# Kernel optimization log

Hardware: AMD Instinct MI355X
Metric: run time of the kernel (lower is better)

The kernel has to match this reference:

```python
import jax, jax.numpy as jnp
import numpy as np

DEPTH = 2
EPS = 1e-12

def _l2norm(x, axis=-1):
    n = jnp.sqrt(jnp.sum(x * x, axis=axis, keepdims=True))
    return x / jnp.maximum(n, EPS)

def setup_inputs() -> dict:
    key = jax.random.key(0)
    k1, k2, k3, k4, k5 = jax.random.split(key, 5)
    N, D, R, E = 50000, 100, 1000, 800000
    features = jax.random.normal(k1, (N, D), dtype=jnp.float32)
    rel_emb = jax.random.normal(k2, (R, D), dtype=jnp.float32)
    none_relation = jax.random.normal(k3, (D,), dtype=jnp.float32)
    # edge list sorted by destination row (matches coalesced sparse layout
    # assumed by the original: softmax values align with edge order)
    rows = jnp.sort(jax.random.randint(k4, (E,), 0, N))
    cols = jax.random.randint(k5, (E,), 0, N)
    adj_index = jnp.stack([rows, cols], axis=1).astype(jnp.int64)
    return {"features": features, "rel_emb": rel_emb,
            "adj_index": adj_index, "none_relation": none_relation}

def reference(features, rel_emb, adj_index, none_relation):
    N = features.shape[0]
    rows = adj_index[:, 0]  # destination (softmax segment, scatter target)
    cols = adj_index[:, 1]  # neighbor (gather source)
    feats = jnp.tanh(features)
    outputs = [feats]
    nr = _l2norm(none_relation, axis=0)  # [D]
    for _ in range(DEPTH):
        neighs = feats[cols]                      # [E, D] gather
        score = -jnp.einsum('ed,d->e', _l2norm(neighs), nr)  # [E]
        # sparse softmax over each destination row's edges
        m = jax.ops.segment_max(score, rows, num_segments=N)
        e = jnp.exp(score - m[rows])
        denom = jax.ops.segment_sum(e, rows, num_segments=N)
        att = e / denom[rows]                     # [E]
        new_feats = jax.ops.segment_sum(neighs * att[:, None], rows,
                                        num_segments=N)  # [N, D]
        feats = jnp.tanh(new_feats)
        outputs.append(feats)
    return jnp.concatenate(outputs, axis=1)  # [N, D*(DEPTH+1)]
```

## Files before the change

kernel.cpp:

```cpp
#include <hip/hip_runtime.h>
#include <hip/hip_fp16.h>
#include <math.h>

#define D_FEAT 100
#define ROW_STRIDE 300
#define ROWB 128u

__device__ __forceinline__ float fast_tanh(float x) {
    float ax = fabsf(x);
    float e  = __expf(2.f * ax);
    float t  = 1.f - 2.f / (e + 1.f);
    return copysignf(t, x);
}

__device__ __forceinline__ unsigned pb4(float x0, float x1, float x2, float x3) {
    unsigned b0 = (unsigned)(int)rintf(fmaf(x0, 127.f, 128.f));
    unsigned b1 = (unsigned)(int)rintf(fmaf(x1, 127.f, 128.f));
    unsigned b2 = (unsigned)(int)rintf(fmaf(x2, 127.f, 128.f));
    unsigned b3 = (unsigned)(int)rintf(fmaf(x3, 127.f, 128.f));
    return b0 | (b1 << 8) | (b2 << 16) | (b3 << 24);
}

__device__ __forceinline__ float half_reduce(float v) {
    #pragma unroll
    for (int off = 16; off; off >>= 1) v += __shfl_xor(v, off, 64);
    return v;
}

__global__ __launch_bounds__(256) void tanh_score_kernel(
    const float* __restrict__ features,
    float* __restrict__ out,
    unsigned char* __restrict__ tab0,
    float* __restrict__ escore0,
    const float* __restrict__ none_rel,
    const int* __restrict__ adj,
    int* __restrict__ startArr,
    int* __restrict__ cols,
    int E, int N)
{
    int gtid = blockIdx.x * blockDim.x + threadIdx.x;
    if (cols && gtid < (E >> 1)) {
        uint4 v = ((const uint4*)adj)[gtid];
        ((int2*)cols)[gtid] = make_int2((int)v.y, (int)v.w);
    }
    if (gtid <= N) {
        if (gtid == N) startArr[N] = E;
        else {
            int lo = 0, hi = E;
            while (lo < hi) {
                int mid = (lo + hi) >> 1;
                if (adj[2 * mid] < gtid) lo = mid + 1; else hi = mid;
            }
            startArr[gtid] = lo;
        }
    }
    if (tab0 && gtid < 8) {
        uint4 z = make_uint4(0x80808080u, 0x80808080u, 0x80808080u, 0x80808080u);
        if (gtid == 7) z.x = 0u;
        *(uint4*)(tab0 + (((size_t)N) << 7) + ((size_t)gtid << 4)) = z;
    }

    int waveId = gtid >> 6;
    int lane = threadIdx.x & 63;
    int h32  = lane >> 5;
    int l    = lane & 31;
    int n    = waveId * 2 + h32;
    const bool valid_n = (n < N);
    const bool fact = valid_n && (l >= 1) && (l <= 25);

    float x0 = 0.f, x1 = 0.f, x2 = 0.f, x3 = 0.f;
    if (fact) {
        float4 f = ((const float4*)(features + (size_t)n * D_FEAT))[l - 1];
        x0 = fast_tanh(f.x); x1 = fast_tanh(f.y);
        x2 = fast_tanh(f.z); x3 = fast_tanh(f.w);
        ((float4*)(out + (size_t)n * ROW_STRIDE))[l - 1] = make_float4(x0, x1, x2, x3);
    }
    unsigned char* row = tab0 ? (tab0 + ((size_t)n << 7)) : nullptr;
    if (row && valid_n) {
        if (l >= 1 && l <= 25) {
            *(unsigned*)(row + 4 * (l - 1)) = pb4(x0, x1, x2, x3);
        } else if (l >= 26 && l != 29) {
            *(unsigned*)(row + 4 * (l - 1)) = 0x80808080u;
        } else if (l == 0) {
            *(unsigned*)(row + 124) = 0x80808080u;
        }
    }

    float nx = 0.f, ny = 0.f, nz = 0.f, nw = 0.f;
    if (l >= 1 && l <= 25) {
        float4 v = ((const float4*)none_rel)[l - 1];
        nx = v.x; ny = v.y; nz = v.z; nw = v.w;
    }
    float ss = half_reduce(nx * nx + ny * ny + nz * nz + nw * nw);
    float inv_nr = 1.f / fmaxf(sqrtf(ss), 1e-12f);

    float dot = half_reduce(x0 * nx + x1 * ny + x2 * nz + x3 * nw) * inv_nr;
    float sq  = half_reduce(x0 * x0 + x1 * x1 + x2 * x2 + x3 * x3);
    if (l == 0 && valid_n) {
        float es = __expf(-dot / fmaxf(sqrtf(sq), 1e-12f));
        escore0[n] = es;
        if (row) *(float*)(row + 112) = es;
    }
}

template <bool WRITE_TAB>
__global__ __launch_bounds__(256) void attn8_kernel(
    const unsigned char* __restrict__ tab,
    float* __restrict__ outp,
    unsigned char* __restrict__ tab_out,
    const int* __restrict__ cols,
    const int* __restrict__ start,
    const float* __restrict__ none_rel,
    int N)
{
    if constexpr (WRITE_TAB) {
        if (blockIdx.x == 0 && threadIdx.x < 8) {
            uint4 z = make_uint4(0x80808080u, 0x80808080u, 0x80808080u, 0x80808080u);
            if (threadIdx.x == 7) z.x = 0u;
            *(uint4*)(tab_out + (((size_t)N) << 7) + ((size_t)threadIdx.x << 4)) = z;
        }
    }

    const int waveId = (int)((blockIdx.x * blockDim.x + threadIdx.x) >> 6);
    const int lane = threadIdx.x & 63;
    const int h32  = lane >> 5;
    const int hl   = lane & 31;
    const int base = h32 << 5;
    const int n    = waveId * 2 + h32;
    const bool valid_n = (n < N);

    const int grp   = hl >> 3;
    const int chunk = hl & 7;
    const unsigned suboff = (unsigned)(chunk << 4);
    const int wl = base + (grp << 3) + 7;

    int e0 = 0, e1 = 0;
    if (valid_n) { e0 = start[n]; e1 = start[n + 1]; }
    const int deg = e1 - e0;
    int maxdeg = deg;
    { int o = __shfl_xor(maxdeg, 32, 64); maxdeg = maxdeg > o ? maxdeg : o; }

    int c0 = N, c1 = N;
    if (hl < deg)      c0 = cols[e0 + hl];
    if (hl + 32 < deg) c1 = cols[e0 + hl + 32];

    float a[16];
    #pragma unroll
    for (int k = 0; k < 16; ++k) a[k] = 0.f;
    float dsum = 0.f;

#define ACC16(V, W)                                                           \
    {                                                                         \
        unsigned _d;                                                          \
        _d = (V).x;                                                           \
        a[0]  = fmaf((float)(_d & 255u),         (W), a[0]);                  \
        a[1]  = fmaf((float)((_d >> 8) & 255u),  (W), a[1]);                  \
        a[2]  = fmaf((float)((_d >> 16) & 255u), (W), a[2]);                  \
        a[3]  = fmaf((float)(_d >> 24),          (W), a[3]);                  \
        _d = (V).y;                                                           \
        a[4]  = fmaf((float)(_d & 255u),         (W), a[4]);                  \
        a[5]  = fmaf((float)((_d >> 8) & 255u),  (W), a[5]);                  \
        a[6]  = fmaf((float)((_d >> 16) & 255u), (W), a[6]);                  \
        a[7]  = fmaf((float)(_d >> 24),          (W), a[7]);                  \
        _d = (V).z;                                                           \
        a[8]  = fmaf((float)(_d & 255u),         (W), a[8]);                  \
        a[9]  = fmaf((float)((_d >> 8) & 255u),  (W), a[9]);                  \
        a[10] = fmaf((float)((_d >> 16) & 255u), (W), a[10]);                 \
        a[11] = fmaf((float)(_d >> 24),          (W), a[11]);                 \
        _d = (V).w;                                                           \
        a[12] = fmaf((float)(_d & 255u),         (W), a[12]);                 \
        a[13] = fmaf((float)((_d >> 8) & 255u),  (W), a[13]);                 \
        a[14] = fmaf((float)((_d >> 16) & 255u), (W), a[14]);                 \
        a[15] = fmaf((float)(_d >> 24),          (W), a[15]);                 \
    }

#define BATCH16(CST, RBASE)                                                   \
    {                                                                         \
        const int sA = base + (RBASE) + grp;                                  \
        int   cA = __shfl((CST), sA,      64), cB = __shfl((CST), sA + 4, 64);\
        int   cC = __shfl((CST), sA + 8,  64), cD = __shfl((CST), sA + 12,64);\
        const uint4 vA = *(const uint4*)(tab + (((size_t)(unsigned)cA) << 7) + suboff); \
        const uint4 vB = *(const uint4*)(tab + (((size_t)(unsigned)cB) << 7) + suboff); \
        const uint4 vC = *(const uint4*)(tab + (((size_t)(unsigned)cC) << 7) + suboff); \
        const uint4 vD = *(const uint4*)(tab + (((size_t)(unsigned)cD) << 7) + suboff); \
        const float wA = __shfl(__uint_as_float(vA.x), wl, 64);               \
        const float wB = __shfl(__uint_as_float(vB.x), wl, 64);               \
        const float wC = __shfl(__uint_as_float(vC.x), wl, 64);               \
        const float wD = __shfl(__uint_as_float(vD.x), wl, 64);               \
        dsum += wA + wB + wC + wD;                                            \
        ACC16(vA, wA) ACC16(vB, wB) ACC16(vC, wC) ACC16(vD, wD)               \
    }

    const int cap1 = maxdeg < 32 ? maxdeg : 32;
    for (int r = 0; r < cap1; r += 16) BATCH16(c0, r)
    const int cap2 = maxdeg < 64 ? maxdeg : 64;
    for (int r = 32; r < cap2; r += 16) BATCH16(c1, r - 32)
#undef BATCH16

    for (int e = e0 + 64; e < e1; ++e) {
        int c = cols[e];
        const uint4 v = *(const uint4*)(tab + (((size_t)(unsigned)c) << 7) + suboff);
        float wv = __shfl(__uint_as_float(v.x), base + 7, 64);
        if (grp == 0) { ACC16(v, wv) dsum += wv; }
    }
#undef ACC16

    #pragma unroll
    for (int k = 0; k < 16; ++k) a[k] += __shfl_xor(a[k], 16, 64);
    #pragma unroll
    for (int k = 0; k < 16; ++k) a[k] += __shfl_xor(a[k], 8, 64);
    dsum += __shfl_xor(dsum, 16, 64);
    dsum += __shfl_xor(dsum, 8, 64);

    const float invd = (deg > 0) ? 1.f / (127.f * dsum) : 0.f;
    const float bsh  = (deg > 0) ? (-128.f / 127.f) : 0.f;
    const int f0 = (chunk << 4) + (grp << 2);
    const bool live = valid_n && (f0 < 100);
    float r0 = 0.f, r1 = 0.f, r2 = 0.f, r3 = 0.f;
    if (live) {
        r0 = fast_tanh(fmaf(a[(grp << 2) + 0], invd, bsh));
        r1 = fast_tanh(fmaf(a[(grp << 2) + 1], invd, bsh));
        r2 = fast_tanh(fmaf(a[(grp << 2) + 2], invd, bsh));
        r3 = fast_tanh(fmaf(a[(grp << 2) + 3], invd, bsh));
    }

    float es = 0.f;
    if constexpr (WRITE_TAB) {
        float n0 = 0.f, n1 = 0.f, n2 = 0.f, n3 = 0.f;
        if (f0 < 100) {
            float4 u = *(const float4*)(none_rel + f0);
            n0 = u.x; n1 = u.y; n2 = u.z; n3 = u.w;
        }
        float ss   = half_reduce(n0*n0 + n1*n1 + n2*n2 + n3*n3);
        float inv_nr = 1.f / fmaxf(sqrtf(ss), 1e-12f);
        float dot  = half_reduce(r0*n0 + r1*n1 + r2*n2 + r3*n3) * inv_nr;
        float sq   = half_reduce(r0*r0 + r1*r1 + r2*r2 + r3*r3);
        es = __expf(-dot / fmaxf(sqrtf(sq), 1e-12f));
    }

    if (live) {
        *(float4*)(outp + (size_t)n * ROW_STRIDE + f0) = make_float4(r0, r1, r2, r3);
    }
    if constexpr (WRITE_TAB) {
        if (valid_n) {
            unsigned word = live ? pb4(r0, r1, r2, r3) : 0x80808080u;
            if (f0 == 112) word = __float_as_uint(es);
            *(unsigned*)(tab_out + ((size_t)n << 7) + (unsigned)f0) = word;
        }
    }
}

__global__ __launch_bounds__(256) void attn_f32_kernel(
    const float* __restrict__ prev,
    float* __restrict__ outp,
    const int2* __restrict__ adj2,
    const int* __restrict__ start,
    const float* __restrict__ escore_in,
    float* __restrict__ escore_out,
    const float* __restrict__ none_rel,
    int N)
{
    int waveId = (int)((blockIdx.x * blockDim.x + threadIdx.x) >> 6);
    int lane = threadIdx.x & 63;
    int h32  = lane >> 5;
    int l    = lane & 31;
    int n    = waveId * 2 + h32;
    const bool valid_n = (n < N);
    const bool fact = valid_n && (l >= 1) && (l <= 25);
    const int base = h32 << 5;

    int e0 = 0, e1 = 0;
    if (valid_n) { e0 = start[n]; e1 = start[n + 1]; }
    const int deg = e1 - e0;

    int   c0 = 0, c1 = 0;
    float w0 = 0.f, w1 = 0.f;
    if (l < deg)      { c0 = adj2[e0 + l].y;      w0 = escore_in[c0]; }
    if (l + 32 < deg) { c1 = adj2[e0 + l + 32].y; w1 = escore_in[c1]; }

    int maxdeg = deg;
    { int o = __shfl_xor(maxdeg, 32, 64); maxdeg = maxdeg > o ? maxdeg : o; }

    float d_acc = 0.f, a0 = 0.f, a1 = 0.f, a2 = 0.f, a3 = 0.f;
    const int cap1 = maxdeg < 32 ? maxdeg : 32;
    for (int r = 0; r < cap1; r += 8) {
        #pragma unroll
        for (int j = 0; j < 8; ++j) {
            int   i = r + j;
            int   c = __shfl(c0, base + i, 64);
            float w = __shfl(w0, base + i, 64);
            float p0 = 0.f, p1 = 0.f, p2 = 0.f, p3 = 0.f;
            if (fact && (i < deg)) {
                float4 v = ((const float4*)(prev + (size_t)c * ROW_STRIDE))[l - 1];
                p0 = v.x; p1 = v.y; p2 = v.z; p3 = v.w;
            }
            if (i >= deg) w = 0.f;
            d_acc += w;
            a0 += w * p0; a1 += w * p1; a2 += w * p2; a3 += w * p3;
        }
    }
    const int cap2 = maxdeg < 64 ? maxdeg : 64;
    for (int r = 32; r < cap2; r += 8) {
        #pragma unroll
        for (int j = 0; j < 8; ++j) {
            int   i = r + j;
            int   c = __shfl(c1, base + i - 32, 64);
            float w = __shfl(w1, base + i - 32, 64);
            float p0 = 0.f, p1 = 0.f, p2 = 0.f, p3 = 0.f;
            if (fact && (i < deg)) {
                float4 v = ((const float4*)(prev + (size_t)c * ROW_STRIDE))[l - 1];
                p0 = v.x; p1 = v.y; p2 = v.z; p3 = v.w;
            }
            if (i >= deg) w = 0.f;
            d_acc += w;
            a0 += w * p0; a1 += w * p1; a2 += w * p2; a3 += w * p3;
        }
    }
    for (int e = e0 + 64; e < e1; ++e) {
        int c = adj2[e].y;
        float w = escore_in[c];
        float p0 = 0.f, p1 = 0.f, p2 = 0.f, p3 = 0.f;
        if (fact) {
            float4 v = ((const float4*)(prev + (size_t)c * ROW_STRIDE))[l - 1];
            p0 = v.x; p1 = v.y; p2 = v.z; p3 = v.w;
        }
        d_acc += w;
        a0 += w * p0; a1 += w * p1; a2 += w * p2; a3 += w * p3;
    }

    const float inv_d = (deg > 0) ? 1.f / d_acc : 0.f;
    float r0 = fast_tanh(a0 * inv_d);
    float r1 = fast_tanh(a1 * inv_d);
    float r2 = fast_tanh(a2 * inv_d);
    float r3 = fast_tanh(a3 * inv_d);
    if (fact) {
        ((float4*)(outp + (size_t)n * ROW_STRIDE))[l - 1] = make_float4(r0, r1, r2, r3);
    } else {
        r0 = r1 = r2 = r3 = 0.f;
    }

    if (escore_out) {
        float nx = 0.f, ny = 0.f, nz = 0.f, nw = 0.f;
        if (l >= 1 && l <= 25) {
            float4 v = ((const float4*)none_rel)[l - 1];
            nx = v.x; ny = v.y; nz = v.z; nw = v.w;
        }
        float ss = half_reduce(nx * nx + ny * ny + nz * nz + nw * nw);
        float inv_nr = 1.f / fmaxf(sqrtf(ss), 1e-12f);
        float dot = half_reduce(r0 * nx + r1 * ny + r2 * nz + r3 * nw) * inv_nr;
        float sq  = half_reduce(r0 * r0 + r1 * r1 + r2 * r2 + r3 * r3);
        if (l == 0 && valid_n) {
            float es = __expf(-dot / fmaxf(sqrtf(sq), 1e-12f));
            escore_out[n] = es;
        }
    }
}

extern "C" void kernel_launch(void* const* d_in, const int* in_sizes, int n_in,
                              void* d_out, int out_size, void* d_ws, size_t ws_size,
                              hipStream_t stream) {
    const float* features = (const float*)d_in[0];
    const int*   adj      = (const int*)d_in[2];
    const float* none_rel = (const float*)d_in[3];
    float* out = (float*)d_out;

    const int N = in_sizes[0] / D_FEAT;
    const int E = in_sizes[2] / 2;

    size_t off = 0;
    auto take = [&](size_t bytes) { size_t o = off; off = (off + bytes + 127) & ~(size_t)127; return o; };
    char* w = (char*)d_ws;
    int*   start   = (int*)  (w + take(sizeof(int)   * (size_t)(N + 1)));
    float* escore0 = (float*)(w + take(sizeof(float) * (size_t)N));
    float* escore1 = (float*)(w + take(sizeof(float) * (size_t)N));
    int*   cols    = (int*)  (w + take(sizeof(int)   * (size_t)E));
    size_t tab_off0 = take((size_t)(N + 1) * ROWB);
    size_t tab_off1 = take((size_t)(N + 1) * ROWB);
    const bool use_tab = (ws_size >= off) &&
                         ((((uintptr_t)w) & 127) == 0);
    unsigned char* tab0 = use_tab ? (unsigned char*)(w + tab_off0) : nullptr;
    unsigned char* tab1 = use_tab ? (unsigned char*)(w + tab_off1) : nullptr;

    const int pairs = (N + 1) / 2;
    const int node_blocks = (pairs * 64 + 255) / 256;
    const int2* adj2 = (const int2*)adj;

    tanh_score_kernel<<<node_blocks, 256, 0, stream>>>(features, out, tab0,
                                                       escore0, none_rel,
                                                       adj, start,
                                                       use_tab ? cols : nullptr,
                                                       E, N);
    if (use_tab) {
        attn8_kernel<true><<<node_blocks, 256, 0, stream>>>(
            tab0, out + D_FEAT, tab1, cols, start, none_rel, N);
        attn8_kernel<false><<<node_blocks, 256, 0, stream>>>(
            tab1, out + 2 * D_FEAT, nullptr, cols, start, none_rel, N);
    } else {
        attn_f32_kernel<<<node_blocks, 256, 0, stream>>>(
            out, out + D_FEAT, adj2, start, escore0, escore1, none_rel, N);
        attn_f32_kernel<<<node_blocks, 256, 0, stream>>>(
            out + D_FEAT, out + 2 * D_FEAT, adj2, start, escore1, nullptr, none_rel, N);
    }
}
```

Baseline: 151.8 us.

## Build row starts from boundary scatter and double-issue gather loads

Row-start offsets are no longer found by a per-node binary search over the sorted edge list. Each thread that already reads a pair of edges now writes the start index for every row boundary that falls inside its pair, and thread 0 fills the leading rows. In the aggregation kernel, the 16-neighbour batches are split into separate load and accumulate steps, so two batches' gathers are in flight before any accumulation. This raises memory-level parallelism at the cost of more live registers.

```diff
diff --git a/kernel.cpp b/kernel.cpp
--- a/kernel.cpp
+++ b/kernel.cpp
@@ -39,20 +39,16 @@
     int E, int N)
 {
     int gtid = blockIdx.x * blockDim.x + threadIdx.x;
-    if (cols && gtid < (E >> 1)) {
+    if (gtid < (E >> 1)) {
         uint4 v = ((const uint4*)adj)[gtid];
-        ((int2*)cols)[gtid] = make_int2((int)v.y, (int)v.w);
-    }
-    if (gtid <= N) {
-        if (gtid == N) startArr[N] = E;
-        else {
-            int lo = 0, hi = E;
-            while (lo < hi) {
-                int mid = (lo + hi) >> 1;
-                if (adj[2 * mid] < gtid) lo = mid + 1; else hi = mid;
-            }
-            startArr[gtid] = lo;
-        }
+        if (cols) ((int2*)cols)[gtid] = make_int2((int)v.y, (int)v.w);
+        const int e  = gtid << 1;
+        const int ra = (int)v.x, rb = (int)v.z;
+        if (gtid == 0)
+            for (int j = 0; j <= ra; ++j) startArr[j] = 0;
+        for (int j = ra + 1; j <= rb; ++j) startArr[j] = e + 1;
+        const int rc = (e + 2 < E) ? adj[2 * (e + 2)] : N;
+        for (int j = rb + 1; j <= rc; ++j) startArr[j] = e + 2;
     }
     if (tab0 && gtid < 8) {
         uint4 z = make_uint4(0x80808080u, 0x80808080u, 0x80808080u, 0x80808080u);
@@ -174,28 +170,52 @@
         a[15] = fmaf((float)(_d >> 24),          (W), a[15]);                 \
     }
 
-#define BATCH16(CST, RBASE)                                                   \
+#define B16_LOAD(CST, RBASE, VA, VB, VC, VD)                                  \
+    uint4 VA, VB, VC, VD;                                                     \
     {                                                                         \
         const int sA = base + (RBASE) + grp;                                  \
-        int   cA = __shfl((CST), sA,      64), cB = __shfl((CST), sA + 4, 64);\
-        int   cC = __shfl((CST), sA + 8,  64), cD = __shfl((CST), sA + 12,64);\
-        const uint4 vA = *(const uint4*)(tab + (((size_t)(unsigned)cA) << 7) + suboff); \
-        const uint4 vB = *(const uint4*)(tab + (((size_t)(unsigned)cB) << 7) + suboff); \
-        const uint4 vC = *(const uint4*)(tab + (((size_t)(unsigned)cC) << 7) + suboff); \
-        const uint4 vD = *(const uint4*)(tab + (((size_t)(unsigned)cD) << 7) + suboff); \
-        const float wA = __shfl(__uint_as_float(vA.x), wl, 64);               \
-        const float wB = __shfl(__uint_as_float(vB.x), wl, 64);               \
-        const float wC = __shfl(__uint_as_float(vC.x), wl, 64);               \
-        const float wD = __shfl(__uint_as_float(vD.x), wl, 64);               \
+        const int cA_ = __shfl((CST), sA,      64);                           \
+        const int cB_ = __shfl((CST), sA + 4,  64);                           \
+        const int cC_ = __shfl((CST), sA + 8,  64);                           \
+        const int cD_ = __shfl((CST), sA + 12, 64);                           \
+        VA = *(const uint4*)(tab + (((size_t)(unsigned)cA_) << 7) + suboff);  \
+        VB = *(const uint4*)(tab + (((size_t)(unsigned)cB_) << 7) + suboff);  \
+        VC = *(const uint4*)(tab + (((size_t)(unsigned)cC_) << 7) + suboff);  \
+        VD = *(const uint4*)(tab + (((size_t)(unsigned)cD_) << 7) + suboff);  \
+    }
+
+#define B16_ACC(VA, VB, VC, VD)                                               \
+    {                                                                         \
+        const float wA = __shfl(__uint_as_float((VA).x), wl, 64);             \
+        const float wB = __shfl(__uint_as_float((VB).x), wl, 64);             \
+        const float wC = __shfl(__uint_as_float((VC).x), wl, 64);             \
+        const float wD = __shfl(__uint_as_float((VD).x), wl, 64);             \
         dsum += wA + wB + wC + wD;                                            \
-        ACC16(vA, wA) ACC16(vB, wB) ACC16(vC, wC) ACC16(vD, wD)               \
-    }
-
-    const int cap1 = maxdeg < 32 ? maxdeg : 32;
-    for (int r = 0; r < cap1; r += 16) BATCH16(c0, r)
-    const int cap2 = maxdeg < 64 ? maxdeg : 64;
-    for (int r = 32; r < cap2; r += 16) BATCH16(c1, r - 32)
-#undef BATCH16
+        ACC16(VA, wA) ACC16(VB, wB) ACC16(VC, wC) ACC16(VD, wD)               \
+    }
+
+    if (maxdeg > 0) {
+        B16_LOAD(c0, 0, va0, va1, va2, va3)
+        if (maxdeg > 16) {
+            B16_LOAD(c0, 16, vb0, vb1, vb2, vb3)
+            B16_ACC(va0, va1, va2, va3)
+            B16_ACC(vb0, vb1, vb2, vb3)
+        } else {
+            B16_ACC(va0, va1, va2, va3)
+        }
+    }
+    if (maxdeg > 32) {
+        B16_LOAD(c1, 0, vc0, vc1, vc2, vc3)
+        if (maxdeg > 48) {
+            B16_LOAD(c1, 16, vd0, vd1, vd2, vd3)
+            B16_ACC(vc0, vc1, vc2, vc3)
+            B16_ACC(vd0, vd1, vd2, vd3)
+        } else {
+            B16_ACC(vc0, vc1, vc2, vc3)
+        }
+    }
+#undef B16_LOAD
+#undef B16_ACC
 
     for (int e = e0 + 64; e < e1; ++e) {
         int c = cols[e];
```

After: 157.1 us. +3.5%, slower.
